# Kernel tuning notes

Hardware: AMD Instinct MI355X
Metric: run time of the kernel (lower is better)

## Reference

```python
import jax, jax.numpy as jnp
import numpy as np

BETA = 0.9
THRESHOLD = 1.0
DELTA_THRESH = 0.2  # spikegen.delta threshold in encoder
NUM_STEPS = 64


def heaviside(v):
    return (v > 0).astype(v.dtype)


def lif_layer(cur):
    """snntorch Leaky (reset_mechanism='subtract') over cur: [S, B, H].
    mem_new = beta*mem + cur - (mem_old > thr)*thr ; spk = (mem_new > thr)."""
    def step(mem, c):
        reset = heaviside(mem - THRESHOLD)
        mem_new = BETA * mem + c - reset * THRESHOLD
        spk = heaviside(mem_new - THRESHOLD)
        return mem_new, spk

    mem0 = jnp.zeros(cur.shape[1:], cur.dtype)
    _, spk_rec = jax.lax.scan(step, mem0, cur)
    return spk_rec  # [S, B, H]


def setup_inputs() -> dict:
    key = jax.random.key(0)
    ks = jax.random.split(key, 7)
    F_in, H1, H2, H3 = 512, 1024, 1024, 512
    x = jax.random.normal(ks[0], (256, 128, F_in), dtype=jnp.float32)
    def lin(k, out_d, in_d):
        kw, kb = jax.random.split(k)
        s = 1.0 / np.sqrt(in_d)
        W = jax.random.uniform(kw, (out_d, in_d), jnp.float32, -s, s)
        b = jax.random.uniform(kb, (out_d,), jnp.float32, -s, s)
        return W, b
    W0, b0 = lin(ks[1], H1, F_in)
    W1, b1 = lin(ks[2], H2, H1)
    W2, b2 = lin(ks[3], H3, H2)
    return {"x": x, "W0": W0, "b0": b0, "W1": W1, "b1": b1, "W2": W2, "b2": b2}


def reference(x, W0, b0, W1, b1, W2, b2):
    B, T, F_in = x.shape
    # SpikeEncoder 'delta': spikegen.delta diffs along dim 0 (batch here, faithful to torch call)
    prev = jnp.concatenate([x[:1], x[:-1]], axis=0)
    delta_spk = ((x - prev) >= DELTA_THRESH).astype(x.dtype)  # [B, T, F]
    # repeat over S then mean over T  ==  mean over T then broadcast over S
    spikes = jnp.broadcast_to(delta_spk.mean(axis=1), (NUM_STEPS, B, F_in))  # [S, B, F]
    for W, b in ((W0, b0), (W1, b1), (W2, b2)):
        cur = jnp.einsum('sbf,hf->sbh', spikes, W) + b  # batched fc across all steps
        spikes = lif_layer(cur)
    return spikes  # [S, B, H_last]
```

## Files before the change

kernel.cpp:

```cpp
#include <hip/hip_runtime.h>
#include <hip/hip_bf16.h>

#define S_STEPS 64

typedef __bf16 bf16x8 __attribute__((ext_vector_type(8)));
typedef float  f32x4  __attribute__((ext_vector_type(4)));
typedef int    i32x4  __attribute__((ext_vector_type(4)));

__device__ __forceinline__ void async16(const void* g, void* l) {
    __builtin_amdgcn_global_load_lds((const __attribute__((address_space(1))) void*)g,
                                     (__attribute__((address_space(3))) void*)l,
                                     16, 0, 0);
}

__global__ void snn_prep(const float4* __restrict__ xv, ushort4* __restrict__ r,
                         const float4* __restrict__ W0, ushort4* __restrict__ w0out,
                         const float4* __restrict__ W1, const float4* __restrict__ W2,
                         char4* __restrict__ w1out, char4* __restrict__ w2out) {
    constexpr int T = 128, F4 = 128;
    constexpr int NB_ENC = 512;
    constexpr int N0_4 = 1024 * 512 / 4;
    constexpr int NB_W0 = N0_4 / 256;
    constexpr int N1_4 = 1024 * 1024 / 4;
    constexpr int N2_4 = 512 * 1024 / 4;
    __shared__ int4 red[4][64];

    const int bid = blockIdx.x;
    if (bid < NB_ENC) {
        const int f4i = threadIdx.x & 63;
        const int tc  = threadIdx.x >> 6;
        const int b   = bid >> 1;
        const int f4  = (bid & 1) * 64 + f4i;
        int c0 = 0, c1 = 0, c2 = 0, c3 = 0;
        if (b > 0) {
            const float4* xb = xv + ((size_t)b * T + tc * 32) * F4 + f4;
            const float4* xp = xb - (size_t)T * F4;
            for (int t = 0; t < 32; ++t) {
                float4 a = xb[(size_t)t * F4];
                float4 p = xp[(size_t)t * F4];
                c0 += (__fsub_rn(a.x, p.x) >= 0.2f) ? 1 : 0;
                c1 += (__fsub_rn(a.y, p.y) >= 0.2f) ? 1 : 0;
                c2 += (__fsub_rn(a.z, p.z) >= 0.2f) ? 1 : 0;
                c3 += (__fsub_rn(a.w, p.w) >= 0.2f) ? 1 : 0;
            }
        }
        red[tc][f4i] = int4{c0, c1, c2, c3};
        __syncthreads();
        if (tc == 0) {
            int4 a = red[0][f4i], bb = red[1][f4i], cc = red[2][f4i], dd = red[3][f4i];
            int s0 = a.x + bb.x + cc.x + dd.x;
            int s1 = a.y + bb.y + cc.y + dd.y;
            int s2 = a.z + bb.z + cc.z + dd.z;
            int s3 = a.w + bb.w + cc.w + dd.w;
            ushort4 o;
            o.x = __hip_bfloat16_raw(__float2bfloat16((float)s0 * (1.0f / 128.0f))).x;
            o.y = __hip_bfloat16_raw(__float2bfloat16((float)s1 * (1.0f / 128.0f))).x;
            o.z = __hip_bfloat16_raw(__float2bfloat16((float)s2 * (1.0f / 128.0f))).x;
            o.w = __hip_bfloat16_raw(__float2bfloat16((float)s3 * (1.0f / 128.0f))).x;
            r[(size_t)b * F4 + f4] = o;
        }
    } else if (bid < NB_ENC + NB_W0) {
        int j = (bid - NB_ENC) * 256 + threadIdx.x;
        float4 w = W0[j];
        float wv[4] = {w.x, w.y, w.z, w.w};
        unsigned short hv[4], mv[4], lv[4];
        #pragma unroll
        for (int q = 0; q < 4; ++q) {
            __hip_bfloat16 hh = __float2bfloat16(wv[q]);
            float r1 = __fsub_rn(wv[q], __bfloat162float(hh));
            __hip_bfloat16 mm = __float2bfloat16(r1);
            float r2 = __fsub_rn(r1, __bfloat162float(mm));
            hv[q] = __hip_bfloat16_raw(hh).x;
            mv[q] = __hip_bfloat16_raw(mm).x;
            lv[q] = __hip_bfloat16_raw(__float2bfloat16(r2)).x;
        }
        w0out[j]             = ushort4{hv[0], hv[1], hv[2], hv[3]};
        w0out[j + N0_4]      = ushort4{mv[0], mv[1], mv[2], mv[3]};
        w0out[j + 2 * N0_4]  = ushort4{lv[0], lv[1], lv[2], lv[3]};
    } else {
        int i = (bid - NB_ENC - NB_W0) * 256 + threadIdx.x;
        const float4* W; char4* out; int n4; int j = i;
        if (j < N1_4) { W = W1; out = w1out; n4 = N1_4; }
        else { j -= N1_4; W = W2; out = w2out; n4 = N2_4; }
        float4 w = W[j];
        float wv[4] = {w.x, w.y, w.z, w.w};
        signed char d2v[4], d1v[4], d0v[4];
        #pragma unroll
        for (int q = 0; q < 4; ++q) {
            int e  = __float2int_rn(wv[q] * 134217728.0f);
            int d0 = (int)(signed char)(e & 0xff);
            int e1 = (e - d0) >> 8;
            int d1 = (int)(signed char)(e1 & 0xff);
            int d2 = (e1 - d1) >> 8;
            d0v[q] = (signed char)d0;
            d1v[q] = (signed char)d1;
            d2v[q] = (signed char)d2;
        }
        out[j]          = make_char4(d2v[0], d2v[1], d2v[2], d2v[3]);
        out[j + n4]     = make_char4(d1v[0], d1v[1], d1v[2], d1v[3]);
        out[j + 2 * n4] = make_char4(d0v[0], d0v[1], d0v[2], d0v[3]);
    }
}


__global__ __launch_bounds__(256, 2)
void snn_gemm_i8_w_lif(const signed char* __restrict__ A,
                       const signed char* __restrict__ Wq,
                       const float* __restrict__ bias,
                       signed char* __restrict__ Sout,
                       int M, int N, int K) {
    __shared__ __align__(16) char As[3 * 8192];
    __shared__ __align__(16) char Bs[3 * 16384];
    const int t    = threadIdx.x;
    const int wave = t >> 6;
    const int lane = t & 63;

    int m_idx, n_idx;
    {
        int gx = gridDim.x, gy = gridDim.y;
        int flat = blockIdx.y * gx + blockIdx.x;
        if ((gy & 7) == 0) {
            int x = flat & 7, local = flat >> 3, h = gy >> 3;
            m_idx = x * h + (local % h);
            n_idx = local / h;
        } else { m_idx = blockIdx.y; n_idx = blockIdx.x; }
    }
    const int m0 = m_idx * 128;
    const int n0 = n_idx * 256;
    const int wm = (wave >> 1) * 64;
    const int wn = (wave & 1) * 128;

    const int srow = lane >> 2;
    const int schk = ((lane & 3) + (lane >> 2) + (lane >> 4)) & 3;
    const int rho  = lane & 15;
    const int kap  = lane >> 4;
    const int foff = ((rho << 2) + ((kap - rho - (rho >> 2)) & 3)) * 16;

    const int KT = K >> 6;
    const int NT = 3 * KT;
    const size_t PK = (size_t)N * K;

    size_t aOff[2], bOff[4];
    #pragma unroll
    for (int q = 0; q < 2; ++q)
        aOff[q] = (size_t)(m0 + (wave * 2 + q) * 16 + srow) * K + schk * 16;
    #pragma unroll
    for (int q = 0; q < 4; ++q)
        bOff[q] = (size_t)(n0 + (wave * 4 + q) * 16 + srow) * K + schk * 16;

    i32x4 acc[4][8] = {};
    i32x4 afA[4], afB[4], bLo[4], bHi[4];

    auto stageT = [&](int p, int kt, int bsel) {
        const int kk = kt << 6;
        char* as = As + bsel * 8192;
        char* bs = Bs + bsel * 16384;
        #pragma unroll
        for (int q = 0; q < 2; ++q)
            async16(A + aOff[q] + kk, as + (wave * 2 + q) * 1024 + lane * 16);
        const signed char* Bw = Wq + (size_t)p * PK;
        #pragma unroll
        for (int q = 0; q < 4; ++q)
            async16(Bw + bOff[q] + kk, bs + (wave * 4 + q) * 1024 + lane * 16);
    };

    int sp = 0, skt = 2;
    int sbuf = 2, rbuf = 1;

    auto body = [&](int i, i32x4* afc, i32x4* afn) {
        if (i + 2 < NT) {
            stageT(sp, skt, sbuf);
            if (++skt == KT) { skt = 0; ++sp; }
            asm volatile("s_waitcnt vmcnt(6)" ::: "memory");
        } else {
            asm volatile("s_waitcnt vmcnt(0)" ::: "memory");
        }
        __builtin_amdgcn_s_barrier();
        const char* as = As + rbuf * 8192;
        const char* bs = Bs + rbuf * 16384;
        #pragma unroll
        for (int q = 0; q < 4; ++q)
            afn[q] = *(const i32x4*)&as[((wm >> 4) + q) * 1024 + foff];
        #pragma unroll
        for (int q = 0; q < 4; ++q)
            bLo[q] = *(const i32x4*)&bs[((wn >> 4) + q) * 1024 + foff];
        __builtin_amdgcn_sched_barrier(0);
        #pragma unroll
        for (int q = 0; q < 4; ++q)
            #pragma unroll
            for (int j = 0; j < 4; ++j)
                acc[q][4 + j] = __builtin_amdgcn_mfma_i32_16x16x64_i8(afc[q], bHi[j], acc[q][4 + j], 0, 0, 0);
        #pragma unroll
        for (int q = 0; q < 4; ++q)
            bHi[q] = *(const i32x4*)&bs[((wn >> 4) + 4 + q) * 1024 + foff];
        asm volatile("s_waitcnt lgkmcnt(0)" ::: "memory");
        __builtin_amdgcn_sched_barrier(0);
        if (((i + 1) & (KT - 1)) == 0) {
            #pragma unroll
            for (int q = 0; q < 4; ++q)
                #pragma unroll
                for (int j = 0; j < 8; ++j)
                    acc[q][j] = acc[q][j] * 256;
        }
        #pragma unroll
        for (int q = 0; q < 4; ++q)
            #pragma unroll
            for (int j = 0; j < 4; ++j)
                acc[q][j] = __builtin_amdgcn_mfma_i32_16x16x64_i8(afn[q], bLo[j], acc[q][j], 0, 0, 0);
        sbuf = (sbuf == 2) ? 0 : sbuf + 1;
        rbuf = (rbuf == 2) ? 0 : rbuf + 1;
    };

    stageT(0, 0, 0);
    stageT(0, 1, 1);
    asm volatile("s_waitcnt vmcnt(6)" ::: "memory");
    __builtin_amdgcn_s_barrier();
    {
        const char* as = As;
        const char* bs = Bs;
        #pragma unroll
        for (int q = 0; q < 4; ++q)
            afA[q] = *(const i32x4*)&as[((wm >> 4) + q) * 1024 + foff];
        #pragma unroll
        for (int q = 0; q < 4; ++q) {
            bLo[q] = *(const i32x4*)&bs[((wn >> 4) + q) * 1024 + foff];
            bHi[q] = *(const i32x4*)&bs[((wn >> 4) + 4 + q) * 1024 + foff];
        }
    }
    asm volatile("s_waitcnt lgkmcnt(0)" ::: "memory");
    __builtin_amdgcn_sched_barrier(0);
    #pragma unroll
    for (int q = 0; q < 4; ++q)
        #pragma unroll
        for (int j = 0; j < 4; ++j)
            acc[q][j] = __builtin_amdgcn_mfma_i32_16x16x64_i8(afA[q], bLo[j], acc[q][j], 0, 0, 0);

    for (int i = 0; i < NT - 2; i += 2) {
        body(i, afA, afB);
        body(i + 1, afB, afA);
    }
    body(NT - 2, afA, afB);
    #pragma unroll
    for (int q = 0; q < 4; ++q)
        #pragma unroll
        for (int j = 0; j < 4; ++j)
            acc[q][4 + j] = __builtin_amdgcn_mfma_i32_16x16x64_i8(afB[q], bHi[j], acc[q][4 + j], 0, 0, 0);

    const float SCALE = 7.450580596923828e-9f;
    float bb[8];
    #pragma unroll
    for (int j = 0; j < 8; ++j)
        bb[j] = bias[n0 + wn + j * 16 + (lane & 15)];
    #pragma unroll
    for (int i = 0; i < 4; ++i)
        #pragma unroll
        for (int j = 0; j < 8; ++j) {
            i32x4 v = acc[i][j];
            f32x4 c;
            #pragma unroll
            for (int r = 0; r < 4; ++r)
                c[r] = (float)v[r] * SCALE + bb[j];
            acc[i][j] = __builtin_bit_cast(i32x4, c);
        }
    float mj[8] = {0.f, 0.f, 0.f, 0.f, 0.f, 0.f, 0.f, 0.f};
    signed char* So = Sout + (size_t)(m0 + wm) * N;
    #pragma unroll
    for (int seg = 0; seg < 16; ++seg) {
        const int si = seg >> 2, sk = seg & 3;
        const int src = (lane & 15) | (((sk + 3) & 3) << 4);
        #pragma unroll
        for (int j = 0; j < 8; ++j) {
            float tin = __shfl(mj[j], src);
            if (seg > 0 && kap == sk) mj[j] = tin;
        }
        if (kap == sk) {
            #pragma unroll
            for (int j = 0; j < 8; ++j) {
                f32x4 c = __builtin_bit_cast(f32x4, acc[si][j]);
                const int ng = n0 + wn + j * 16 + (lane & 15);
                #pragma unroll
                for (int r = 0; r < 4; ++r) {
                    float rst = (mj[j] > 1.0f) ? 1.0f : 0.0f;
                    mj[j] = __fsub_rn(__fadd_rn(__fmul_rn(0.9f, mj[j]), c[r]), rst);
                    So[(size_t)(seg * 4 + r) * N + ng] = (mj[j] > 1.0f) ? (signed char)1 : (signed char)0;
                }
            }
        }
    }
}

__global__ __launch_bounds__(256, 2)
void snn_gemm_i8_n_lif(const signed char* __restrict__ A,
                       const signed char* __restrict__ Wq,
                       const float* __restrict__ bias,
                       float* __restrict__ Dout,
                       int M, int N, int K, int Bsz) {
    __shared__ __align__(16) char As[3 * 8192];
    __shared__ __align__(16) char Bs[3 * 8192];
    const int t    = threadIdx.x;
    const int wave = t >> 6;
    const int lane = t & 63;

    int m_idx, n_idx;
    {
        int gx = gridDim.x, gy = gridDim.y;
        int flat = blockIdx.y * gx + blockIdx.x;
        if ((gy & 7) == 0) {
            int x = flat & 7, local = flat >> 3, h = gy >> 3;
            m_idx = x * h + (local % h);
            n_idx = local / h;
        } else { m_idx = blockIdx.y; n_idx = blockIdx.x; }
    }
    const int m0 = m_idx * 128;
    const int n0 = n_idx * 128;
    const int wm = (wave & 1) * 64;
    const int wn = (wave >> 1) * 64;

    const int srow = lane >> 2;
    const int schk = ((lane & 3) + (lane >> 2) + (lane >> 4)) & 3;
    const int rho  = lane & 15;
    const int kap  = lane >> 4;
    const int foff = ((rho << 2) + ((kap - rho - (rho >> 2)) & 3)) * 16;

    const int KT = K >> 6;
    const int NT = 3 * KT;
    const size_t PK = (size_t)N * K;

    size_t aOff[2], bOff[2];
    #pragma unroll
    for (int q = 0; q < 2; ++q) {
        aOff[q] = (size_t)(m0 + (wave * 2 + q) * 16 + srow) * K + schk * 16;
        bOff[q] = (size_t)(n0 + (wave * 2 + q) * 16 + srow) * K + schk * 16;
    }

    i32x4 acc[4][4] = {};
    i32x4 afA[4], afB[4], bLo[2], bHi[2];

    auto stageT = [&](int p, int kt, int bsel) {
        const int kk = kt << 6;
        char* as = As + bsel * 8192;
        char* bs = Bs + bsel * 8192;
        const signed char* Bw = Wq + (size_t)p * PK;
        #pragma unroll
        for (int q = 0; q < 2; ++q) {
            async16(A  + aOff[q] + kk, as + (wave * 2 + q) * 1024 + lane * 16);
            async16(Bw + bOff[q] + kk, bs + (wave * 2 + q) * 1024 + lane * 16);
        }
    };

    int sp = 0, skt = 2;
    int sbuf = 2, rbuf = 1;

    auto body = [&](int i, i32x4* afc, i32x4* afn) {
        if (i + 2 < NT) {
            stageT(sp, skt, sbuf);
            if (++skt == KT) { skt = 0; ++sp; }
            asm volatile("s_waitcnt vmcnt(4)" ::: "memory");
        } else {
            asm volatile("s_waitcnt vmcnt(0)" ::: "memory");
        }
        __builtin_amdgcn_s_barrier();
        const char* as = As + rbuf * 8192;
        const char* bs = Bs + rbuf * 8192;
        #pragma unroll
        for (int q = 0; q < 4; ++q)
            afn[q] = *(const i32x4*)&as[((wm >> 4) + q) * 1024 + foff];
        #pragma unroll
        for (int q = 0; q < 2; ++q)
            bLo[q] = *(const i32x4*)&bs[((wn >> 4) + q) * 1024 + foff];
        __builtin_amdgcn_sched_barrier(0);
        #pragma unroll
        for (int q = 0; q < 4; ++q)
            #pragma unroll
            for (int j = 0; j < 2; ++j)
                acc[q][2 + j] = __builtin_amdgcn_mfma_i32_16x16x64_i8(afc[q], bHi[j], acc[q][2 + j], 0, 0, 0);
        #pragma unroll
        for (int q = 0; q < 2; ++q)
            bHi[q] = *(const i32x4*)&bs[((wn >> 4) + 2 + q) * 1024 + foff];
        asm volatile("s_waitcnt lgkmcnt(0)" ::: "memory");
        __builtin_amdgcn_sched_barrier(0);
        if (((i + 1) & (KT - 1)) == 0) {
            #pragma unroll
            for (int q = 0; q < 4; ++q)
                #pragma unroll
                for (int j = 0; j < 4; ++j)
                    acc[q][j] = acc[q][j] * 256;
        }
        #pragma unroll
        for (int q = 0; q < 4; ++q)
            #pragma unroll
            for (int j = 0; j < 2; ++j)
                acc[q][j] = __builtin_amdgcn_mfma_i32_16x16x64_i8(afn[q], bLo[j], acc[q][j], 0, 0, 0);
        sbuf = (sbuf == 2) ? 0 : sbuf + 1;
        rbuf = (rbuf == 2) ? 0 : rbuf + 1;
    };

    stageT(0, 0, 0);
    stageT(0, 1, 1);
    asm volatile("s_waitcnt vmcnt(4)" ::: "memory");
    __builtin_amdgcn_s_barrier();
    {
        const char* as = As;
        const char* bs = Bs;
        #pragma unroll
        for (int q = 0; q < 4; ++q)
            afA[q] = *(const i32x4*)&as[((wm >> 4) + q) * 1024 + foff];
        #pragma unroll
        for (int q = 0; q < 2; ++q) {
            bLo[q] = *(const i32x4*)&bs[((wn >> 4) + q) * 1024 + foff];
            bHi[q] = *(const i32x4*)&bs[((wn >> 4) + 2 + q) * 1024 + foff];
        }
    }
    asm volatile("s_waitcnt lgkmcnt(0)" ::: "memory");
    __builtin_amdgcn_sched_barrier(0);
    #pragma unroll
    for (int q = 0; q < 4; ++q)
        #pragma unroll
        for (int j = 0; j < 2; ++j)
            acc[q][j] = __builtin_amdgcn_mfma_i32_16x16x64_i8(afA[q], bLo[j], acc[q][j], 0, 0, 0);

    for (int i = 0; i < NT - 2; i += 2) {
        body(i, afA, afB);
        body(i + 1, afB, afA);
    }
    body(NT - 2, afA, afB);
    #pragma unroll
    for (int q = 0; q < 4; ++q)
        #pragma unroll
        for (int j = 0; j < 2; ++j)
            acc[q][2 + j] = __builtin_amdgcn_mfma_i32_16x16x64_i8(afB[q], bHi[j], acc[q][2 + j], 0, 0, 0);

    const float SCALE = 7.450580596923828e-9f;
    float bb[4];
    #pragma unroll
    for (int j = 0; j < 4; ++j)
        bb[j] = bias[n0 + wn + j * 16 + (lane & 15)];
    #pragma unroll
    for (int i = 0; i < 4; ++i)
        #pragma unroll
        for (int j = 0; j < 4; ++j) {
            i32x4 v = acc[i][j];
            f32x4 c;
            #pragma unroll
            for (int r = 0; r < 4; ++r)
                c[r] = (float)v[r] * SCALE + bb[j];
            acc[i][j] = __builtin_bit_cast(i32x4, c);
        }
    float mj[4] = {0.f, 0.f, 0.f, 0.f};
    const int b_idx = (m0 + wm) >> 6;
    #pragma unroll
    for (int seg = 0; seg < 16; ++seg) {
        const int si = seg >> 2, sk = seg & 3;
        const int src = (lane & 15) | (((sk + 3) & 3) << 4);
        #pragma unroll
        for (int j = 0; j < 4; ++j) {
            float tin = __shfl(mj[j], src);
            if (seg > 0 && kap == sk) mj[j] = tin;
        }
        if (kap == sk) {
            #pragma unroll
            for (int j = 0; j < 4; ++j) {
                f32x4 c = __builtin_bit_cast(f32x4, acc[si][j]);
                const int ng = n0 + wn + j * 16 + (lane & 15);
                #pragma unroll
                for (int r = 0; r < 4; ++r) {
                    float rst = (mj[j] > 1.0f) ? 1.0f : 0.0f;
                    mj[j] = __fsub_rn(__fadd_rn(__fmul_rn(0.9f, mj[j]), c[r]), rst);
                    Dout[((size_t)(seg * 4 + r) * Bsz + b_idx) * N + ng] = (mj[j] > 1.0f) ? 1.0f : 0.0f;
                }
            }
        }
    }
}

__global__ __launch_bounds__(256)
void snn_gemm_mfma_n(const __hip_bfloat16* __restrict__ A,
                     const __hip_bfloat16* __restrict__ Whi,
                     const __hip_bfloat16* __restrict__ Wmid,
                     const __hip_bfloat16* __restrict__ Wlo,
                     const float* __restrict__ bias,
                     float* __restrict__ C,
                     int M, int N, int K) {
    __shared__ __align__(16) unsigned short As[128 * 32];
    __shared__ __align__(16) unsigned short Bs[128 * 32];
    const int t    = threadIdx.x;
    const int wave = t >> 6;
    const int lane = t & 63;

    int m_idx = blockIdx.y, n_idx = blockIdx.x;
    const int m0 = m_idx * 128;
    const int n0 = n_idx * 128;
    const int wm = (wave & 1) * 64;
    const int wn = (wave >> 1) * 64;

    const int srow = lane >> 2;
    const int schk = ((lane & 3) + (lane >> 2) + (lane >> 4)) & 3;
    const int rho  = lane & 15;
    const int kap  = lane >> 4;
    const int foff = ((rho << 2) + ((kap - rho - (rho >> 2)) & 3)) * 8;

    f32x4 acc[4][4] = {};

    const __hip_bfloat16* parts[3] = {Whi, Wmid, Wlo};
    for (int part = 0; part < 3; ++part) {
        const __hip_bfloat16* Bw = parts[part];
        for (int k0 = 0; k0 < K; k0 += 32) {
            __syncthreads();
            #pragma unroll
            for (int q = 0; q < 2; ++q) {
                int grp = wave * 2 + q;
                async16(A  + (size_t)(m0 + grp * 16 + srow) * K + k0 + schk * 8,
                        &As[grp * 512 + lane * 8]);
                async16(Bw + (size_t)(n0 + grp * 16 + srow) * K + k0 + schk * 8,
                        &Bs[grp * 512 + lane * 8]);
            }
            __syncthreads();

            bf16x8 af[4], bfr[4];
            #pragma unroll
            for (int i = 0; i < 4; ++i) {
                af[i]  = *(const bf16x8*)&As[((wm >> 4) + i) * 512 + foff];
                bfr[i] = *(const bf16x8*)&Bs[((wn >> 4) + i) * 512 + foff];
            }
            #pragma unroll
            for (int i = 0; i < 4; ++i)
                #pragma unroll
                for (int j = 0; j < 4; ++j)
                    acc[i][j] = __builtin_amdgcn_mfma_f32_16x16x32_bf16(af[i], bfr[j], acc[i][j], 0, 0, 0);
        }
    }

    #pragma unroll
    for (int i = 0; i < 4; ++i) {
        int mg = m0 + wm + i * 16 + (lane >> 4) * 4;
        #pragma unroll
        for (int j = 0; j < 4; ++j) {
            int ng = n0 + wn + j * 16 + (lane & 15);
            float bb = bias[ng];
            #pragma unroll
            for (int r = 0; r < 4; ++r)
                C[(size_t)(mg + r) * N + ng] = acc[i][j][r] + bb;
        }
    }
}

__global__ void snn_lif0_i8_bmaj(const float4* __restrict__ cur, uchar4* __restrict__ spk,
                                 int BH4, int H4) {
    int idx = blockIdx.x * blockDim.x + threadIdx.x;
    if (idx >= BH4) return;
    const int b  = idx / H4;
    const int h4 = idx - b * H4;
    uchar4* out = spk + (size_t)b * S_STEPS * H4 + h4;
    float m0 = 0.0f, m1 = 0.0f, m2 = 0.0f, m3 = 0.0f;
    float4 c = cur[idx];
    for (int s = 0; s < S_STEPS; ++s) {
        float r0 = (m0 > 1.0f) ? 1.0f : 0.0f;
        float r1 = (m1 > 1.0f) ? 1.0f : 0.0f;
        float r2 = (m2 > 1.0f) ? 1.0f : 0.0f;
        float r3 = (m3 > 1.0f) ? 1.0f : 0.0f;
        m0 = __fsub_rn(__fadd_rn(__fmul_rn(0.9f, m0), c.x), r0);
        m1 = __fsub_rn(__fadd_rn(__fmul_rn(0.9f, m1), c.y), r1);
        m2 = __fsub_rn(__fadd_rn(__fmul_rn(0.9f, m2), c.z), r2);
        m3 = __fsub_rn(__fadd_rn(__fmul_rn(0.9f, m3), c.w), r3);
        uchar4 o;
        o.x = (m0 > 1.0f) ? 1 : 0;
        o.y = (m1 > 1.0f) ? 1 : 0;
        o.z = (m2 > 1.0f) ? 1 : 0;
        o.w = (m3 > 1.0f) ? 1 : 0;
        out[(size_t)s * H4] = o;
    }
}

extern "C" void kernel_launch(void* const* d_in, const int* in_sizes, int n_in,
                              void* d_out, int out_size, void* d_ws, size_t ws_size,
                              hipStream_t stream) {
    const float* x  = (const float*)d_in[0];
    const float* W0 = (const float*)d_in[1];
    const float* b0 = (const float*)d_in[2];
    const float* W1 = (const float*)d_in[3];
    const float* b1 = (const float*)d_in[4];
    const float* W2 = (const float*)d_in[5];
    const float* b2 = (const float*)d_in[6];

    const int B = 256, T = 128, F = 512, H1 = 1024, H2 = 1024, H3 = 512;
    const int SB = S_STEPS * B;

    char* w = (char*)d_ws;
    signed char*    spk0 = (signed char*)w;                 w += (size_t)SB * H1;
    signed char*    spk1 = (signed char*)w;                 w += (size_t)SB * H2;
    __hip_bfloat16* r_bf = (__hip_bfloat16*)w;              w += (size_t)B * F * 2;
    float*          cur0 = (float*)w;                       w += (size_t)B * H1 * 4;
    __hip_bfloat16* W0s  = (__hip_bfloat16*)w;              w += (size_t)3 * H1 * F * 2;
    signed char*    W1q  = (signed char*)w;                 w += (size_t)3 * H2 * H1;
    signed char*    W2q  = (signed char*)w;                 w += (size_t)3 * H3 * H2;

    const int nW0 = H1 * F;

    snn_prep<<<dim3(2560), dim3(256), 0, stream>>>(
        (const float4*)x, (ushort4*)r_bf,
        (const float4*)W0, (ushort4*)W0s,
        (const float4*)W1, (const float4*)W2,
        (char4*)W1q, (char4*)W2q);

    snn_gemm_mfma_n<<<dim3(H1 / 128, B / 128), dim3(256), 0, stream>>>(
        r_bf, W0s, W0s + nW0, W0s + 2 * nW0, b0, cur0, B, H1, F);

    snn_lif0_i8_bmaj<<<dim3(B * H1 / 4 / 256), dim3(256), 0, stream>>>(
        (const float4*)cur0, (uchar4*)spk0, B * H1 / 4, H1 / 4);

    snn_gemm_i8_w_lif<<<dim3(H2 / 256, SB / 128), dim3(256), 0, stream>>>(
        spk0, W1q, b1, spk1, SB, H2, H1);

    snn_gemm_i8_n_lif<<<dim3(H3 / 128, SB / 128), dim3(256), 0, stream>>>(
        spk1, W2q, b2, (float*)d_out, SB, H3, H2, B);
}
```

Baseline: 254.2 us.

## Split layer-0 GEMM over weight parts and triple-buffer its K loop

The layer-0 bf16 GEMM previously looped serially over three weight parts (hi/mid/lo) in a single 16-block grid. It now launches a third grid dimension over the parts, each writing a partial output, and uses a triple-buffered async LDS pipeline with interleaved fragment loads and MFMAs. The LIF kernel then sums the three partials plus bias before the recurrence. This adds parallelism and hides load latency, at the cost of extra partial-output traffic and a changed summation order.

```diff
diff --git a/kernel.cpp b/kernel.cpp
--- a/kernel.cpp
+++ b/kernel.cpp
@@ -473,23 +473,23 @@
     }
 }
 
-__global__ __launch_bounds__(256)
-void snn_gemm_mfma_n(const __hip_bfloat16* __restrict__ A,
-                     const __hip_bfloat16* __restrict__ Whi,
-                     const __hip_bfloat16* __restrict__ Wmid,
-                     const __hip_bfloat16* __restrict__ Wlo,
-                     const float* __restrict__ bias,
-                     float* __restrict__ C,
-                     int M, int N, int K) {
-    __shared__ __align__(16) unsigned short As[128 * 32];
-    __shared__ __align__(16) unsigned short Bs[128 * 32];
+__global__ __launch_bounds__(256, 2)
+void snn_gemm0_bf16p(const __hip_bfloat16* __restrict__ A,
+                     const __hip_bfloat16* __restrict__ Wp,
+                     float* __restrict__ Cpart) {
+    constexpr int M = 256, N = 1024, K = 512;
+    constexpr int KT = K / 32;
+    __shared__ __align__(16) char As[3 * 8192];
+    __shared__ __align__(16) char Bs[3 * 8192];
     const int t    = threadIdx.x;
     const int wave = t >> 6;
     const int lane = t & 63;
 
-    int m_idx = blockIdx.y, n_idx = blockIdx.x;
-    const int m0 = m_idx * 128;
-    const int n0 = n_idx * 128;
+    const int part = blockIdx.z;
+    const __hip_bfloat16* Bw = Wp + (size_t)part * N * K;
+    float* C = Cpart + (size_t)part * M * N;
+    const int m0 = blockIdx.y * 128;
+    const int n0 = blockIdx.x * 128;
     const int wm = (wave & 1) * 64;
     const int wn = (wave >> 1) * 64;
 
@@ -497,38 +497,103 @@
     const int schk = ((lane & 3) + (lane >> 2) + (lane >> 4)) & 3;
     const int rho  = lane & 15;
     const int kap  = lane >> 4;
-    const int foff = ((rho << 2) + ((kap - rho - (rho >> 2)) & 3)) * 8;
+    const int foff = ((rho << 2) + ((kap - rho - (rho >> 2)) & 3)) * 16;
+
+    size_t aOff[2], bOff[2];
+    #pragma unroll
+    for (int q = 0; q < 2; ++q) {
+        aOff[q] = (size_t)(m0 + (wave * 2 + q) * 16 + srow) * K + schk * 8;
+        bOff[q] = (size_t)(n0 + (wave * 2 + q) * 16 + srow) * K + schk * 8;
+    }
 
     f32x4 acc[4][4] = {};
-
-    const __hip_bfloat16* parts[3] = {Whi, Wmid, Wlo};
-    for (int part = 0; part < 3; ++part) {
-        const __hip_bfloat16* Bw = parts[part];
-        for (int k0 = 0; k0 < K; k0 += 32) {
-            __syncthreads();
-            #pragma unroll
-            for (int q = 0; q < 2; ++q) {
-                int grp = wave * 2 + q;
-                async16(A  + (size_t)(m0 + grp * 16 + srow) * K + k0 + schk * 8,
-                        &As[grp * 512 + lane * 8]);
-                async16(Bw + (size_t)(n0 + grp * 16 + srow) * K + k0 + schk * 8,
-                        &Bs[grp * 512 + lane * 8]);
-            }
-            __syncthreads();
-
-            bf16x8 af[4], bfr[4];
-            #pragma unroll
-            for (int i = 0; i < 4; ++i) {
-                af[i]  = *(const bf16x8*)&As[((wm >> 4) + i) * 512 + foff];
-                bfr[i] = *(const bf16x8*)&Bs[((wn >> 4) + i) * 512 + foff];
-            }
-            #pragma unroll
-            for (int i = 0; i < 4; ++i)
-                #pragma unroll
-                for (int j = 0; j < 4; ++j)
-                    acc[i][j] = __builtin_amdgcn_mfma_f32_16x16x32_bf16(af[i], bfr[j], acc[i][j], 0, 0, 0);
-        }
-    }
+    bf16x8 afA[4], afB[4], bLo[2], bHi[2];
+
+    auto stageT = [&](int kt, int bsel) {
+        const int kk = kt << 5;
+        char* as = As + bsel * 8192;
+        char* bs = Bs + bsel * 8192;
+        #pragma unroll
+        for (int q = 0; q < 2; ++q) {
+            async16(A  + aOff[q] + kk, as + (wave * 2 + q) * 1024 + lane * 16);
+            async16(Bw + bOff[q] + kk, bs + (wave * 2 + q) * 1024 + lane * 16);
+        }
+    };
+
+    int skt = 2;
+    int sbuf = 2, rbuf = 1;
+
+    auto body = [&](int i, bf16x8* afc, bf16x8* afn) {
+        if (i + 2 < KT) {
+            stageT(skt, sbuf);
+            ++skt;
+            asm volatile("s_waitcnt vmcnt(4)" ::: "memory");
+        } else {
+            asm volatile("s_waitcnt vmcnt(0)" ::: "memory");
+        }
+        __builtin_amdgcn_s_barrier();
+        const char* as = As + rbuf * 8192;
+        const char* bs = Bs + rbuf * 8192;
+        #pragma unroll
+        for (int q = 0; q < 4; ++q)
+            afn[q] = *(const bf16x8*)&as[((wm >> 4) + q) * 1024 + foff];
+        #pragma unroll
+        for (int q = 0; q < 2; ++q)
+            bLo[q] = *(const bf16x8*)&bs[((wn >> 4) + q) * 1024 + foff];
+        __builtin_amdgcn_sched_barrier(0);
+        #pragma unroll
+        for (int q = 0; q < 4; ++q)
+            #pragma unroll
+            for (int j = 0; j < 2; ++j)
+                acc[q][2 + j] = __builtin_amdgcn_mfma_f32_16x16x32_bf16(afc[q], bHi[j], acc[q][2 + j], 0, 0, 0);
+        #pragma unroll
+        for (int q = 0; q < 2; ++q)
+            bHi[q] = *(const bf16x8*)&bs[((wn >> 4) + 2 + q) * 1024 + foff];
+        asm volatile("s_waitcnt lgkmcnt(0)" ::: "memory");
+        __builtin_amdgcn_sched_barrier(0);
+        #pragma unroll
+        for (int q = 0; q < 4; ++q)
+            #pragma unroll
+            for (int j = 0; j < 2; ++j)
+                acc[q][j] = __builtin_amdgcn_mfma_f32_16x16x32_bf16(afn[q], bLo[j], acc[q][j], 0, 0, 0);
+        sbuf = (sbuf == 2) ? 0 : sbuf + 1;
+        rbuf = (rbuf == 2) ? 0 : rbuf + 1;
+    };
+
+    stageT(0, 0);
+    stageT(1, 1);
+    asm volatile("s_waitcnt vmcnt(4)" ::: "memory");
+    __builtin_amdgcn_s_barrier();
+    {
+        const char* as = As;
+        const char* bs = Bs;
+        #pragma unroll
+        for (int q = 0; q < 4; ++q)
+            afA[q] = *(const bf16x8*)&as[((wm >> 4) + q) * 1024 + foff];
+        #pragma unroll
+        for (int q = 0; q < 2; ++q) {
+            bLo[q] = *(const bf16x8*)&bs[((wn >> 4) + q) * 1024 + foff];
+            bHi[q] = *(const bf16x8*)&bs[((wn >> 4) + 2 + q) * 1024 + foff];
+        }
+    }
+    asm volatile("s_waitcnt lgkmcnt(0)" ::: "memory");
+    __builtin_amdgcn_sched_barrier(0);
+    #pragma unroll
+    for (int q = 0; q < 4; ++q)
+        #pragma unroll
+        for (int j = 0; j < 2; ++j)
+            acc[q][j] = __builtin_amdgcn_mfma_f32_16x16x32_bf16(afA[q], bLo[j], acc[q][j], 0, 0, 0);
+
+    for (int i = 0; i < KT - 2; i += 2) {
+        body(i, afA, afB);
+        body(i + 1, afB, afA);
+    }
+    body(KT - 2, afA, afB);
+    #pragma unroll
+    for (int q = 0; q < 4; ++q)
+        #pragma unroll
+        for (int j = 0; j < 2; ++j)
+            acc[q][2 + j] = __builtin_amdgcn_mfma_f32_16x16x32_bf16(afB[q], bHi[j], acc[q][2 + j], 0, 0, 0);
 
     #pragma unroll
     for (int i = 0; i < 4; ++i) {
@@ -536,23 +601,29 @@
         #pragma unroll
         for (int j = 0; j < 4; ++j) {
             int ng = n0 + wn + j * 16 + (lane & 15);
-            float bb = bias[ng];
             #pragma unroll
             for (int r = 0; r < 4; ++r)
-                C[(size_t)(mg + r) * N + ng] = acc[i][j][r] + bb;
+                C[(size_t)(mg + r) * N + ng] = acc[i][j][r];
         }
     }
 }
 
-__global__ void snn_lif0_i8_bmaj(const float4* __restrict__ cur, uchar4* __restrict__ spk,
-                                 int BH4, int H4) {
+__global__ void snn_lif0_sum3(const float4* __restrict__ p, const float4* __restrict__ b4,
+                              uchar4* __restrict__ spk) {
+    constexpr int MN4 = 256 * 1024 / 4;
+    constexpr int H4  = 256;
     int idx = blockIdx.x * blockDim.x + threadIdx.x;
-    if (idx >= BH4) return;
-    const int b  = idx / H4;
-    const int h4 = idx - b * H4;
+    if (idx >= MN4) return;
+    const int b  = idx >> 8;
+    const int h4 = idx & 255;
+    float4 h = p[idx], mm = p[idx + MN4], l = p[idx + 2 * MN4], bb = b4[h4];
+    float4 c;
+    c.x = __fadd_rn(__fadd_rn(__fadd_rn(h.x, mm.x), l.x), bb.x);
+    c.y = __fadd_rn(__fadd_rn(__fadd_rn(h.y, mm.y), l.y), bb.y);
+    c.z = __fadd_rn(__fadd_rn(__fadd_rn(h.z, mm.z), l.z), bb.z);
+    c.w = __fadd_rn(__fadd_rn(__fadd_rn(h.w, mm.w), l.w), bb.w);
     uchar4* out = spk + (size_t)b * S_STEPS * H4 + h4;
     float m0 = 0.0f, m1 = 0.0f, m2 = 0.0f, m3 = 0.0f;
-    float4 c = cur[idx];
     for (int s = 0; s < S_STEPS; ++s) {
         float r0 = (m0 > 1.0f) ? 1.0f : 0.0f;
         float r1 = (m1 > 1.0f) ? 1.0f : 0.0f;
@@ -589,12 +660,10 @@
     signed char*    spk0 = (signed char*)w;                 w += (size_t)SB * H1;
     signed char*    spk1 = (signed char*)w;                 w += (size_t)SB * H2;
     __hip_bfloat16* r_bf = (__hip_bfloat16*)w;              w += (size_t)B * F * 2;
-    float*          cur0 = (float*)w;                       w += (size_t)B * H1 * 4;
+    float*          cur0p = (float*)w;                      w += (size_t)3 * B * H1 * 4;
     __hip_bfloat16* W0s  = (__hip_bfloat16*)w;              w += (size_t)3 * H1 * F * 2;
     signed char*    W1q  = (signed char*)w;                 w += (size_t)3 * H2 * H1;
     signed char*    W2q  = (signed char*)w;                 w += (size_t)3 * H3 * H2;
-
-    const int nW0 = H1 * F;
 
     snn_prep<<<dim3(2560), dim3(256), 0, stream>>>(
         (const float4*)x, (ushort4*)r_bf,
@@ -602,11 +671,11 @@
         (const float4*)W1, (const float4*)W2,
         (char4*)W1q, (char4*)W2q);
 
-    snn_gemm_mfma_n<<<dim3(H1 / 128, B / 128), dim3(256), 0, stream>>>(
-        r_bf, W0s, W0s + nW0, W0s + 2 * nW0, b0, cur0, B, H1, F);
-
-    snn_lif0_i8_bmaj<<<dim3(B * H1 / 4 / 256), dim3(256), 0, stream>>>(
-        (const float4*)cur0, (uchar4*)spk0, B * H1 / 4, H1 / 4);
+    snn_gemm0_bf16p<<<dim3(H1 / 128, B / 128, 3), dim3(256), 0, stream>>>(
+        r_bf, W0s, cur0p);
+
+    snn_lif0_sum3<<<dim3(B * H1 / 4 / 256), dim3(256), 0, stream>>>(
+        (const float4*)cur0p, (const float4*)b0, (uchar4*)spk0);
 
     snn_gemm_i8_w_lif<<<dim3(H2 / 256, SB / 128), dim3(256), 0, stream>>>(
         spk0, W1q, b1, spk1, SB, H2, H1);
```

Result: faster. 233.1 us (-8.3%).
